# Performance work log

Measured on AMD Instinct MI355X. Metric: run time of the kernel, lower is better.

Reference implementation:

```python
import jax, jax.numpy as jnp
import numpy as np

D = 1024      # input_dim / hidden_size
H = 16        # n_heads
HD = D // H   # head_size = 64
F = 4096      # mlp_dim
EPS = 1e-6


def setup_inputs() -> dict:
    key = jax.random.key(0)
    ks = jax.random.split(key, 16)
    s = 0.02
    inp = {
        "x": jax.random.normal(ks[0], (4, 2048, D), dtype=jnp.float32),
        # attention params (torch Linear: y = x @ W.T + b; we store W as [out,in])
        "Wq": jax.random.normal(ks[1], (D, D), dtype=jnp.float32) * s,
        "bq": jax.random.normal(ks[2], (D,), dtype=jnp.float32) * s,
        "Wk": jax.random.normal(ks[3], (D, D), dtype=jnp.float32) * s,
        "bk": jax.random.normal(ks[4], (D,), dtype=jnp.float32) * s,
        "Wv": jax.random.normal(ks[5], (D, D), dtype=jnp.float32) * s,
        "bv": jax.random.normal(ks[6], (D,), dtype=jnp.float32) * s,
        "Wo": jax.random.normal(ks[7], (D, D), dtype=jnp.float32) * s,
        "bo": jax.random.normal(ks[8], (D,), dtype=jnp.float32) * s,
        # MLP params
        "W1": jax.random.normal(ks[9], (F, D), dtype=jnp.float32) * s,
        "b1": jax.random.normal(ks[10], (F,), dtype=jnp.float32) * s,
        "W2": jax.random.normal(ks[11], (D, F), dtype=jnp.float32) * s,
        "b2": jax.random.normal(ks[12], (D,), dtype=jnp.float32) * s,
        # LayerNorm params
        "ln1_g": jnp.ones((D,), dtype=jnp.float32),
        "ln1_b": jnp.zeros((D,), dtype=jnp.float32),
        "ln2_g": jnp.ones((D,), dtype=jnp.float32),
        "ln2_b": jnp.zeros((D,), dtype=jnp.float32),
    }
    return inp


def _layernorm(x, g, b):
    mu = jnp.mean(x, axis=-1, keepdims=True)
    var = jnp.mean(jnp.square(x - mu), axis=-1, keepdims=True)
    return (x - mu) * jax.lax.rsqrt(var + EPS) * g + b


def reference(x, Wq, bq, Wk, bk, Wv, bv, Wo, bo, W1, b1, W2, b2,
              ln1_g, ln1_b, ln2_g, ln2_b):
    B, S, _ = x.shape
    h = x
    xn = _layernorm(x, ln1_g, ln1_b)
    # Q/K/V projections -> [B, H, S, HD]
    def split_heads(t):
        return t.reshape(B, S, H, HD).transpose(0, 2, 1, 3)
    q = split_heads(xn @ Wq.T + bq)
    k = split_heads(xn @ Wk.T + bk)
    v = split_heads(xn @ Wv.T + bv)
    scores = jnp.einsum('bhqd,bhkd->bhqk', q, k) / np.sqrt(HD).astype(np.float32)
    probs = jax.nn.softmax(scores, axis=-1)
    ctx = jnp.einsum('bhqk,bhkd->bhqd', probs, v)      # [B,H,S,HD]
    ctx = ctx.transpose(0, 2, 1, 3).reshape(B, S, D)
    attn_out = ctx @ Wo.T + bo
    x = attn_out + h
    h = x
    xn = _layernorm(x, ln2_g, ln2_b)
    y = jax.nn.gelu(xn @ W1.T + b1, approximate=False)  # torch nn.GELU() = exact erf gelu
    y = y @ W2.T + b2
    return y + h
```

## Files before the change

### kernel.cpp

```cpp
#include <hip/hip_runtime.h>
#include <hip/hip_bf16.h>
#include <math.h>

typedef __attribute__((ext_vector_type(8))) short short8;
typedef __attribute__((ext_vector_type(4))) float f32x4;

#define MFMA_BF16 __builtin_amdgcn_mfma_f32_16x16x32_bf16

__device__ __forceinline__ ushort f2bf(float f) {
  union { __hip_bfloat16 h; ushort u; } c;
  c.h = __float2bfloat16(f);
  return c.u;
}
__device__ __forceinline__ void async_cp16(const ushort* g, ushort* l) {
  __builtin_amdgcn_global_load_lds(
      (const __attribute__((address_space(1))) void*)g,
      (__attribute__((address_space(3))) void*)l, 16, 0, 0);
}

__global__ __launch_bounds__(256) void conv_all(
    const float* __restrict__ Wq, const float* __restrict__ Wk,
    const float* __restrict__ Wv, const float* __restrict__ Wo,
    const float* __restrict__ W1, const float* __restrict__ W2,
    const float* __restrict__ bq, const float* __restrict__ bk,
    const float* __restrict__ bv,
    ushort* __restrict__ wqkv, ushort* __restrict__ wo,
    ushort* __restrict__ w1, ushort* __restrict__ w2,
    float* __restrict__ bqkv) {
  int i = blockIdx.x * 256 + threadIdx.x;
  if (i < 3145728) {
    const float* src; ushort* dst; int off;
    if (i < 786432)        {
      dst = wqkv; off = i;
      if (i < 262144)      src = Wq + (size_t)i * 4;
      else if (i < 524288) src = Wk + (size_t)(i - 262144) * 4;
      else                 src = Wv + (size_t)(i - 524288) * 4;
    } else if (i < 1048576) { dst = wo; off = i - 786432;  src = Wo + (size_t)off * 4; }
    else if (i < 2097152)   { dst = w1; off = i - 1048576; src = W1 + (size_t)off * 4; }
    else                    { dst = w2; off = i - 2097152; src = W2 + (size_t)off * 4; }
    float4 v = *(const float4*)src;
    ushort4 o;
    o.x = f2bf(v.x); o.y = f2bf(v.y); o.z = f2bf(v.z); o.w = f2bf(v.w);
    ((ushort4*)dst)[off] = o;
  } else if (i < 3146496) {
    int off = i - 3145728;
    const float* src;
    if (off < 256)      src = bq + (size_t)off * 4;
    else if (off < 512) src = bk + (size_t)(off - 256) * 4;
    else                src = bv + (size_t)(off - 512) * 4;
    ((float4*)bqkv)[off] = *(const float4*)src;
  }
}

__global__ __launch_bounds__(256) void ln_kernel(const float* __restrict__ x,
    const float* __restrict__ g, const float* __restrict__ b,
    ushort* __restrict__ out) {
  const int row = blockIdx.x, t = threadIdx.x;
  float4 v = ((const float4*)(x + (size_t)row * 1024))[t];
  float s  = v.x + v.y + v.z + v.w;
  float ss = v.x*v.x + v.y*v.y + v.z*v.z + v.w*v.w;
  #pragma unroll
  for (int off = 32; off >= 1; off >>= 1) {
    s  += __shfl_xor(s, off);
    ss += __shfl_xor(ss, off);
  }
  __shared__ float red[8];
  int wv = t >> 6, ln = t & 63;
  if (ln == 0) { red[wv] = s; red[4 + wv] = ss; }
  __syncthreads();
  float S  = red[0] + red[1] + red[2] + red[3];
  float SS = red[4] + red[5] + red[6] + red[7];
  float mu  = S * (1.0f/1024.0f);
  float var = SS * (1.0f/1024.0f) - mu*mu;
  float rs  = rsqrtf(var + 1e-6f);
  float4 gv = ((const float4*)g)[t];
  float4 bv = ((const float4*)b)[t];
  ushort4 o;
  o.x = f2bf((v.x-mu)*rs*gv.x + bv.x);
  o.y = f2bf((v.y-mu)*rs*gv.y + bv.y);
  o.z = f2bf((v.z-mu)*rs*gv.z + bv.z);
  o.w = f2bf((v.w-mu)*rs*gv.w + bv.w);
  ((ushort4*)(out + (size_t)row*1024))[t] = o;
}

enum { EPI_QK = 0, EPI_VT = 1, EPI_WO = 2, EPI_GELU = 3, EPI_OUT = 4 };

template <int EPI>
__global__ __launch_bounds__(256) void gemm_kernel(const ushort* __restrict__ A,
    const ushort* __restrict__ Bw, const float* __restrict__ bias,
    const float* __restrict__ res, void* __restrict__ outp,
    void* __restrict__ outp2, int K, int N, float scale) {
  __shared__ ushort As[2][128 * 32];
  __shared__ ushort Bs[2][128 * 32];
  const int t = threadIdx.x;
  const int m0 = blockIdx.x * 128, n0 = blockIdx.y * 128;
  const int lane = t & 63, wave = t >> 6;
  const int col = lane & 15, quad = lane >> 4;
  const int wrow = (wave >> 1) * 64, wcol = (wave & 1) * 64;

  f32x4 acc[4][4];
  #pragma unroll
  for (int i = 0; i < 4; i++)
    #pragma unroll
    for (int j = 0; j < 4; j++)
      acc[i][j] = (f32x4){0.f, 0.f, 0.f, 0.f};

  const int lrow = lane >> 2, lcol = (lane & 3) * 8;
  const ushort* Ag = A  + (size_t)(m0 + wave * 32 + lrow) * K + lcol;
  const ushort* Bg = Bw + (size_t)(n0 + wave * 32 + lrow) * K + lcol;
  const int ldso = (wave * 32) * 32;

  for (int k0 = 0; k0 < K; k0 += 64) {
    __syncthreads();
    #pragma unroll
    for (int c = 0; c < 2; c++) {
      async_cp16(Ag + k0 + c * 32,                  &As[c][ldso]);
      async_cp16(Ag + (size_t)16 * K + k0 + c * 32, &As[c][ldso + 16 * 32]);
      async_cp16(Bg + k0 + c * 32,                  &Bs[c][ldso]);
      async_cp16(Bg + (size_t)16 * K + k0 + c * 32, &Bs[c][ldso + 16 * 32]);
    }
    __syncthreads();
    #pragma unroll
    for (int c = 0; c < 2; c++) {
      short8 af[4], bf[4];
      #pragma unroll
      for (int tm = 0; tm < 4; tm++)
        af[tm] = *(const short8*)&As[c][(wrow + tm * 16 + col) * 32 + quad * 8];
      #pragma unroll
      for (int tn = 0; tn < 4; tn++)
        bf[tn] = *(const short8*)&Bs[c][(wcol + tn * 16 + col) * 32 + quad * 8];
      #pragma unroll
      for (int tm = 0; tm < 4; tm++)
        #pragma unroll
        for (int tn = 0; tn < 4; tn++)
          acc[tm][tn] = MFMA_BF16(af[tm], bf[tn], acc[tm][tn], 0, 0, 0);
    }
  }

  #pragma unroll
  for (int tm = 0; tm < 4; tm++) {
    #pragma unroll
    for (int tn = 0; tn < 4; tn++) {
      const int n = n0 + wcol + tn * 16 + col;
      const float bn = (EPI == EPI_VT) ? 0.f : bias[n];
      #pragma unroll
      for (int r = 0; r < 4; r++) {
        const int m = m0 + wrow + tm * 16 + quad * 4 + r;
        float v = acc[tm][tn][r] + bn;
        if (EPI == EPI_VT) {
          float vv = v + bias[m];
          int h = m >> 6, hd = m & 63, bb = n >> 11, s2 = n & 2047;
          ((ushort*)outp)[((size_t)((bb * 16 + h) * 64 + hd)) * 2048 + s2] = f2bf(vv);
        } else if (EPI == EPI_GELU) {
          float u = v * 0.7978845608028654f * (1.0f + 0.044715f * v * v);
          float e = __builtin_amdgcn_exp2f(u * 2.885390081777927f);
          float th = 1.0f - 2.0f * __builtin_amdgcn_rcpf(e + 1.0f);
          ((ushort*)outp)[(size_t)m * N + n] = f2bf(0.5f * v * (1.0f + th));
        } else {
          ((float*)outp)[(size_t)m * N + n] = v + res[(size_t)m * N + n];
        }
      }
    }
  }
}

template <int EPI>
__global__ __launch_bounds__(512, 2) void gemm256_kernel(const ushort* __restrict__ A,
    const ushort* __restrict__ Bw, const float* __restrict__ bias,
    void* __restrict__ outp, void* __restrict__ outp2, int K, int N, float scale) {
  __shared__ ushort As[2][256 * 64];
  __shared__ ushort Bs[2][256 * 64];
  const int t = threadIdx.x;
  const int lane = t & 63, wave = t >> 6;
  const int col = lane & 15, quad = lane >> 4;
  const int m0 = blockIdx.x * 256, n0 = blockIdx.y * 256;
  const int wm = wave >> 2, wn = wave & 3;

  f32x4 acc[8][4];
  #pragma unroll
  for (int i = 0; i < 8; i++)
    #pragma unroll
    for (int j = 0; j < 4; j++)
      acc[i][j] = (f32x4){0.f, 0.f, 0.f, 0.f};

  size_t aoff[4], boff[4];
  int sdst[4];
  #pragma unroll
  for (int i = 0; i < 4; i++) {
    int c = i * 512 + t;
    int row = c >> 3, p = c & 7;
    int gcol = (p ^ (row & 7)) * 8;
    aoff[i] = (size_t)(m0 + row) * K + gcol;
    boff[i] = (size_t)(n0 + row) * K + gcol;
    sdst[i] = c * 8;
  }

  const int NT = K >> 6;
  #pragma unroll
  for (int i = 0; i < 4; i++) {
    async_cp16(A  + aoff[i], &As[0][sdst[i]]);
    async_cp16(Bw + boff[i], &Bs[0][sdst[i]]);
  }

  int cur = 0;
  for (int kt = 0; kt < NT; kt++) {
    if (kt + 1 < NT) {
      const int nxt = cur ^ 1;
      const int ko = (kt + 1) << 6;
      #pragma unroll
      for (int i = 0; i < 4; i++) {
        async_cp16(A  + aoff[i] + ko, &As[nxt][sdst[i]]);
        async_cp16(Bw + boff[i] + ko, &Bs[nxt][sdst[i]]);
      }
      asm volatile("s_waitcnt vmcnt(8)" ::: "memory");
    } else {
      asm volatile("s_waitcnt vmcnt(0)" ::: "memory");
    }
    __builtin_amdgcn_sched_barrier(0);
    __builtin_amdgcn_s_barrier();
    __builtin_amdgcn_sched_barrier(0);

    #pragma unroll
    for (int c = 0; c < 2; c++) {
      short8 af[8], bf[4];
      #pragma unroll
      for (int tm = 0; tm < 8; tm++) {
        const int row = wm * 128 + tm * 16 + col;
        af[tm] = *(const short8*)&As[cur][row * 64 + ((c * 4 + quad) ^ (row & 7)) * 8];
      }
      #pragma unroll
      for (int tn = 0; tn < 4; tn++) {
        const int row = wn * 64 + tn * 16 + col;
        bf[tn] = *(const short8*)&Bs[cur][row * 64 + ((c * 4 + quad) ^ (row & 7)) * 8];
      }
      __builtin_amdgcn_s_setprio(1);
      #pragma unroll
      for (int tm = 0; tm < 8; tm++)
        #pragma unroll
        for (int tn = 0; tn < 4; tn++)
          acc[tm][tn] = MFMA_BF16(af[tm], bf[tn], acc[tm][tn], 0, 0, 0);
      __builtin_amdgcn_s_setprio(0);
    }

    asm volatile("s_waitcnt lgkmcnt(0)" ::: "memory");
    __builtin_amdgcn_sched_barrier(0);
    __builtin_amdgcn_s_barrier();
    cur ^= 1;
  }

  #pragma unroll
  for (int tm = 0; tm < 8; tm++) {
    #pragma unroll
    for (int tn = 0; tn < 4; tn++) {
      const int n = n0 + wn * 64 + tn * 16 + col;
      const float bn = bias[n];
      #pragma unroll
      for (int r = 0; r < 4; r++) {
        const int m = m0 + wm * 128 + tm * 16 + quad * 4 + r;
        float v = acc[tm][tn][r] + bn;
        if (EPI == EPI_QK) {
          int nl = n & 1023, h = nl >> 6, hd = nl & 63;
          int bb = m >> 11, s2 = m & 2047;
          if (n < 1024)
            ((ushort*)outp)[(((size_t)(bb * 16 + h) * 2048 + s2) * 64) + hd] = f2bf(v * scale);
          else
            ((ushort*)outp2)[(((size_t)(bb * 16 + h) * 2048 + s2) * 64) + hd] = f2bf(v);
        } else {
          float u = v * 0.7978845608028654f * (1.0f + 0.044715f * v * v);
          float e = __builtin_amdgcn_exp2f(u * 2.885390081777927f);
          float th = 1.0f - 2.0f * __builtin_amdgcn_rcpf(e + 1.0f);
          ((ushort*)outp)[(size_t)m * N + n] = f2bf(0.5f * v * (1.0f + th));
        }
      }
    }
  }
}

__global__ __launch_bounds__(256) void attn_kernel(const ushort* __restrict__ Qb,
    const ushort* __restrict__ Kb, const ushort* __restrict__ Vt,
    ushort* __restrict__ ctx) {
  const int lane = threadIdx.x & 63, wave = threadIdx.x >> 6;
  const int col = lane & 15, quad = lane >> 4;
  const int bx = blockIdx.x;
  const int bh = bx & 63;
  const int qt = bx >> 6;
  const int qbase = qt * 128 + wave * 32;
  const ushort* Qh = Qb + (size_t)bh * 2048 * 64;
  const ushort* Kh = Kb + (size_t)bh * 2048 * 64;
  const ushort* Vh = Vt + (size_t)bh * 64 * 2048;

  short8 qa[2][2];
  #pragma unroll
  for (int qg = 0; qg < 2; qg++) {
    const ushort* Qr = Qh + (size_t)(qbase + qg * 16 + col) * 64 + quad * 8;
    qa[qg][0] = *(const short8*)Qr;
    qa[qg][1] = *(const short8*)(Qr + 32);
  }

  f32x4 Ot[2][4];
  float l_part[2];
  #pragma unroll
  for (int qg = 0; qg < 2; qg++) {
    l_part[qg] = 0.f;
    #pragma unroll
    for (int dt = 0; dt < 4; dt++) Ot[qg][dt] = (f32x4){0.f, 0.f, 0.f, 0.f};
  }

  __shared__ ushort Ks[2][2][64 * 32];
  __shared__ ushort Vs[2][2][64 * 32];
  __shared__ ushort P_lds[4][2][16][64];

  const int lrow = lane >> 2;
  const int srow = wave * 16 + lrow;
  const int lcol = ((lane & 3) ^ ((srow >> 1) & 3)) * 8;
  const ushort* Kg = Kh + (size_t)srow * 64 + lcol;
  const ushort* Vg = Vh + (size_t)srow * 2048 + lcol;
  const int so = (wave * 16) * 32;

  const int kvswz = (col >> 1) & 3;
  const int pswz = col & 7;

  async_cp16(Kg,      &Ks[0][0][so]);
  async_cp16(Kg + 32, &Ks[0][1][so]);
  async_cp16(Vg,      &Vs[0][0][so]);
  async_cp16(Vg + 32, &Vs[0][1][so]);
  __syncthreads();

  int cur = 0;
  for (int kb = 0; kb < 2048; kb += 64) {
    if (kb + 64 < 2048) {
      const int nxt = cur ^ 1;
      async_cp16(Kg + (size_t)(kb + 64) * 64,      &Ks[nxt][0][so]);
      async_cp16(Kg + (size_t)(kb + 64) * 64 + 32, &Ks[nxt][1][so]);
      async_cp16(Vg + (kb + 64),                   &Vs[nxt][0][so]);
      async_cp16(Vg + (kb + 64) + 32,              &Vs[nxt][1][so]);
    }

    short8 kf[4][2], vf[4][2];
    #pragma unroll
    for (int kt = 0; kt < 4; kt++)
      #pragma unroll
      for (int c = 0; c < 2; c++)
        kf[kt][c] = *(const short8*)&Ks[cur][c][(kt * 16 + col) * 32 + (quad ^ kvswz) * 8];
    #pragma unroll
    for (int dt = 0; dt < 4; dt++)
      #pragma unroll
      for (int c = 0; c < 2; c++)
        vf[dt][c] = *(const short8*)&Vs[cur][c][(dt * 16 + col) * 32 + (quad ^ kvswz) * 8];

    #pragma unroll
    for (int qg = 0; qg < 2; qg++) {
      f32x4 s[4];
      __builtin_amdgcn_s_setprio(1);
      #pragma unroll
      for (int kt = 0; kt < 4; kt++) {
        s[kt] = (f32x4){0.f, 0.f, 0.f, 0.f};
        s[kt] = MFMA_BF16(kf[kt][0], qa[qg][0], s[kt], 0, 0, 0);
        s[kt] = MFMA_BF16(kf[kt][1], qa[qg][1], s[kt], 0, 0, 0);
      }
      __builtin_amdgcn_s_setprio(0);
      ushort(*P)[64] = P_lds[wave][qg];
      #pragma unroll
      for (int kt = 0; kt < 4; kt++) {
        float p0 = __builtin_amdgcn_exp2f(s[kt][0]);
        float p1 = __builtin_amdgcn_exp2f(s[kt][1]);
        float p2 = __builtin_amdgcn_exp2f(s[kt][2]);
        float p3 = __builtin_amdgcn_exp2f(s[kt][3]);
        l_part[qg] += (p0 + p1) + (p2 + p3);
        uint2 pk;
        asm("v_cvt_pk_bf16_f32 %0, %1, %2" : "=v"(pk.x) : "v"(p0), "v"(p1));
        asm("v_cvt_pk_bf16_f32 %0, %1, %2" : "=v"(pk.y) : "v"(p2), "v"(p3));
        *(uint2*)&P[col][(((2 * kt + (quad >> 1)) ^ pswz) * 8) + (quad & 1) * 4] = pk;
      }
    }
    #pragma unroll
    for (int qg = 0; qg < 2; qg++) {
      #pragma unroll
      for (int c = 0; c < 2; c++) {
        short8 pf = *(const short8*)&P_lds[wave][qg][col][((4 * c + quad) ^ pswz) * 8];
        __builtin_amdgcn_s_setprio(1);
        #pragma unroll
        for (int dt = 0; dt < 4; dt++)
          Ot[qg][dt] = MFMA_BF16(vf[dt][c], pf, Ot[qg][dt], 0, 0, 0);
        __builtin_amdgcn_s_setprio(0);
      }
    }
    __syncthreads();
    cur ^= 1;
  }

  const int bb = bh >> 4, h = bh & 15;
  #pragma unroll
  for (int qg = 0; qg < 2; qg++) {
    float l = l_part[qg];
    l += __shfl_xor(l, 16);
    l += __shfl_xor(l, 32);
    float inv = __builtin_amdgcn_rcpf(l);
    const int q = qbase + qg * 16 + col;
    size_t base = ((size_t)(bb * 2048 + q)) * 1024 + h * 64;
    #pragma unroll
    for (int dt = 0; dt < 4; dt++) {
      ushort4 o;
      o.x = f2bf(Ot[qg][dt][0] * inv);
      o.y = f2bf(Ot[qg][dt][1] * inv);
      o.z = f2bf(Ot[qg][dt][2] * inv);
      o.w = f2bf(Ot[qg][dt][3] * inv);
      *(ushort4*)&ctx[base + dt * 16 + quad * 4] = o;
    }
  }
}

extern "C" void kernel_launch(void* const* d_in, const int* in_sizes, int n_in,
                              void* d_out, int out_size, void* d_ws, size_t ws_size,
                              hipStream_t stream) {
  const float* x     = (const float*)d_in[0];
  const float* Wq    = (const float*)d_in[1];
  const float* bq    = (const float*)d_in[2];
  const float* Wk    = (const float*)d_in[3];
  const float* bk    = (const float*)d_in[4];
  const float* Wv    = (const float*)d_in[5];
  const float* bv    = (const float*)d_in[6];
  const float* Wo    = (const float*)d_in[7];
  const float* bo    = (const float*)d_in[8];
  const float* W1    = (const float*)d_in[9];
  const float* b1    = (const float*)d_in[10];
  const float* W2    = (const float*)d_in[11];
  const float* b2    = (const float*)d_in[12];
  const float* ln1_g = (const float*)d_in[13];
  const float* ln1_b = (const float*)d_in[14];
  const float* ln2_g = (const float*)d_in[15];
  const float* ln2_b = (const float*)d_in[16];

  const size_t MB = 1ull << 20;
  char* ws = (char*)d_ws;
  ushort* Wqkv_b = (ushort*)(ws + 0 * MB);
  ushort* Wo_b   = (ushort*)(ws + 6 * MB);
  ushort* W1_b   = (ushort*)(ws + 8 * MB);
  ushort* W2_b   = (ushort*)(ws + 16 * MB);
  ushort* xn1    = (ushort*)(ws + 24 * MB);
  ushort* Qb     = (ushort*)(ws + 40 * MB);
  ushort* Kb     = (ushort*)(ws + 56 * MB);
  ushort* Vt     = (ushort*)(ws + 72 * MB);
  ushort* ctxb   = (ushort*)(ws + 88 * MB);
  float*  x2     = (float*)(ws + 104 * MB);
  ushort* xn2    = (ushort*)(ws + 136 * MB);
  ushort* y1     = (ushort*)(ws + 152 * MB);
  float*  bqkv   = (float*)(ws + 152 * MB);

  conv_all<<<12291, 256, 0, stream>>>(Wq, Wk, Wv, Wo, W1, W2, bq, bk, bv,
                                      Wqkv_b, Wo_b, W1_b, W2_b, bqkv);

  ln_kernel<<<8192, 256, 0, stream>>>(x, ln1_g, ln1_b, xn1);

  const float cs = 0.125f * 1.4426950408889634f;
  gemm256_kernel<EPI_QK><<<dim3(32, 8), 512, 0, stream>>>(
      xn1, Wqkv_b, bqkv, Qb, Kb, 1024, 2048, cs);
  gemm_kernel<EPI_VT><<<dim3(8, 64), 256, 0, stream>>>(
      Wqkv_b + (size_t)2048 * 1024, xn1, bqkv + 2048, nullptr, Vt, nullptr,
      1024, 8192, 1.0f);

  attn_kernel<<<1024, 256, 0, stream>>>(Qb, Kb, Vt, ctxb);

  gemm_kernel<EPI_WO><<<dim3(64, 8), 256, 0, stream>>>(
      ctxb, Wo_b, bo, x, x2, nullptr, 1024, 1024, 1.0f);

  ln_kernel<<<8192, 256, 0, stream>>>(x2, ln2_g, ln2_b, xn2);

  gemm256_kernel<EPI_GELU><<<dim3(32, 16), 512, 0, stream>>>(
      xn2, W1_b, b1, y1, nullptr, 1024, 4096, 1.0f);
  gemm_kernel<EPI_OUT><<<dim3(64, 8), 256, 0, stream>>>(
      y1, W2_b, b2, x2, d_out, nullptr, 4096, 1024, 1.0f);
}
```

Baseline: 515.2 us.

## Replace 128x128 GEMMs with pipelined 256x128 tile kernel; load V directly from global

Adds a new 512-thread GEMM kernel with a 256x128 tile, XOR-swizzled LDS layout, double buffering that issues the next tile's async loads before computing the current one, and explicit waitcnt/barrier scheduling. It replaces the older 128x128 single-stage kernel for the V projection, the Wo projection and the W2 down-projection. The aim is more reuse per loaded byte and overlap of global loads with MFMA work. Separately, the attention kernel stops staging V through LDS and reads V fragments straight from global memory. That saves LDS traffic and barriers but risks global-load latency on the critical path.

```diff
diff --git a/kernel.cpp b/kernel.cpp
--- a/kernel.cpp
+++ b/kernel.cpp
@@ -86,85 +86,6 @@
 enum { EPI_QK = 0, EPI_VT = 1, EPI_WO = 2, EPI_GELU = 3, EPI_OUT = 4 };
 
 template <int EPI>
-__global__ __launch_bounds__(256) void gemm_kernel(const ushort* __restrict__ A,
-    const ushort* __restrict__ Bw, const float* __restrict__ bias,
-    const float* __restrict__ res, void* __restrict__ outp,
-    void* __restrict__ outp2, int K, int N, float scale) {
-  __shared__ ushort As[2][128 * 32];
-  __shared__ ushort Bs[2][128 * 32];
-  const int t = threadIdx.x;
-  const int m0 = blockIdx.x * 128, n0 = blockIdx.y * 128;
-  const int lane = t & 63, wave = t >> 6;
-  const int col = lane & 15, quad = lane >> 4;
-  const int wrow = (wave >> 1) * 64, wcol = (wave & 1) * 64;
-
-  f32x4 acc[4][4];
-  #pragma unroll
-  for (int i = 0; i < 4; i++)
-    #pragma unroll
-    for (int j = 0; j < 4; j++)
-      acc[i][j] = (f32x4){0.f, 0.f, 0.f, 0.f};
-
-  const int lrow = lane >> 2, lcol = (lane & 3) * 8;
-  const ushort* Ag = A  + (size_t)(m0 + wave * 32 + lrow) * K + lcol;
-  const ushort* Bg = Bw + (size_t)(n0 + wave * 32 + lrow) * K + lcol;
-  const int ldso = (wave * 32) * 32;
-
-  for (int k0 = 0; k0 < K; k0 += 64) {
-    __syncthreads();
-    #pragma unroll
-    for (int c = 0; c < 2; c++) {
-      async_cp16(Ag + k0 + c * 32,                  &As[c][ldso]);
-      async_cp16(Ag + (size_t)16 * K + k0 + c * 32, &As[c][ldso + 16 * 32]);
-      async_cp16(Bg + k0 + c * 32,                  &Bs[c][ldso]);
-      async_cp16(Bg + (size_t)16 * K + k0 + c * 32, &Bs[c][ldso + 16 * 32]);
-    }
-    __syncthreads();
-    #pragma unroll
-    for (int c = 0; c < 2; c++) {
-      short8 af[4], bf[4];
-      #pragma unroll
-      for (int tm = 0; tm < 4; tm++)
-        af[tm] = *(const short8*)&As[c][(wrow + tm * 16 + col) * 32 + quad * 8];
-      #pragma unroll
-      for (int tn = 0; tn < 4; tn++)
-        bf[tn] = *(const short8*)&Bs[c][(wcol + tn * 16 + col) * 32 + quad * 8];
-      #pragma unroll
-      for (int tm = 0; tm < 4; tm++)
-        #pragma unroll
-        for (int tn = 0; tn < 4; tn++)
-          acc[tm][tn] = MFMA_BF16(af[tm], bf[tn], acc[tm][tn], 0, 0, 0);
-    }
-  }
-
-  #pragma unroll
-  for (int tm = 0; tm < 4; tm++) {
-    #pragma unroll
-    for (int tn = 0; tn < 4; tn++) {
-      const int n = n0 + wcol + tn * 16 + col;
-      const float bn = (EPI == EPI_VT) ? 0.f : bias[n];
-      #pragma unroll
-      for (int r = 0; r < 4; r++) {
-        const int m = m0 + wrow + tm * 16 + quad * 4 + r;
-        float v = acc[tm][tn][r] + bn;
-        if (EPI == EPI_VT) {
-          float vv = v + bias[m];
-          int h = m >> 6, hd = m & 63, bb = n >> 11, s2 = n & 2047;
-          ((ushort*)outp)[((size_t)((bb * 16 + h) * 64 + hd)) * 2048 + s2] = f2bf(vv);
-        } else if (EPI == EPI_GELU) {
-          float u = v * 0.7978845608028654f * (1.0f + 0.044715f * v * v);
-          float e = __builtin_amdgcn_exp2f(u * 2.885390081777927f);
-          float th = 1.0f - 2.0f * __builtin_amdgcn_rcpf(e + 1.0f);
-          ((ushort*)outp)[(size_t)m * N + n] = f2bf(0.5f * v * (1.0f + th));
-        } else {
-          ((float*)outp)[(size_t)m * N + n] = v + res[(size_t)m * N + n];
-        }
-      }
-    }
-  }
-}
-
-template <int EPI>
 __global__ __launch_bounds__(512, 2) void gemm256_kernel(const ushort* __restrict__ A,
     const ushort* __restrict__ Bw, const float* __restrict__ bias,
     void* __restrict__ outp, void* __restrict__ outp2, int K, int N, float scale) {
@@ -276,6 +197,114 @@
   }
 }
 
+template <int EPI>
+__global__ __launch_bounds__(512, 2) void gemmBig_kernel(const ushort* __restrict__ A,
+    const ushort* __restrict__ Bw, const float* __restrict__ bias,
+    const float* __restrict__ res, void* __restrict__ outp, int K, int N) {
+  __shared__ ushort As[2][256 * 64];
+  __shared__ ushort Bs[2][128 * 64];
+  const int t = threadIdx.x;
+  const int lane = t & 63, wave = t >> 6;
+  const int col = lane & 15, quad = lane >> 4;
+  const int m0 = blockIdx.x * 256, n0 = blockIdx.y * 128;
+  const int wm = wave >> 1, wn = wave & 1;
+
+  f32x4 acc[4][4];
+  #pragma unroll
+  for (int i = 0; i < 4; i++)
+    #pragma unroll
+    for (int j = 0; j < 4; j++)
+      acc[i][j] = (f32x4){0.f, 0.f, 0.f, 0.f};
+
+  size_t aoff[4], boff[2];
+  int adst[4], bdst[2];
+  #pragma unroll
+  for (int i = 0; i < 4; i++) {
+    int c = i * 512 + t;
+    int row = c >> 3, p = c & 7;
+    aoff[i] = (size_t)(m0 + row) * K + (p ^ (row & 7)) * 8;
+    adst[i] = c * 8;
+  }
+  #pragma unroll
+  for (int i = 0; i < 2; i++) {
+    int c = i * 512 + t;
+    int row = c >> 3, p = c & 7;
+    boff[i] = (size_t)(n0 + row) * K + (p ^ (row & 7)) * 8;
+    bdst[i] = c * 8;
+  }
+
+  const int NT = K >> 6;
+  #pragma unroll
+  for (int i = 0; i < 4; i++) async_cp16(A + aoff[i], &As[0][adst[i]]);
+  #pragma unroll
+  for (int i = 0; i < 2; i++) async_cp16(Bw + boff[i], &Bs[0][bdst[i]]);
+
+  int cur = 0;
+  for (int kt = 0; kt < NT; kt++) {
+    if (kt + 1 < NT) {
+      const int nxt = cur ^ 1;
+      const int ko = (kt + 1) << 6;
+      #pragma unroll
+      for (int i = 0; i < 4; i++) async_cp16(A + aoff[i] + ko, &As[nxt][adst[i]]);
+      #pragma unroll
+      for (int i = 0; i < 2; i++) async_cp16(Bw + boff[i] + ko, &Bs[nxt][bdst[i]]);
+      asm volatile("s_waitcnt vmcnt(6)" ::: "memory");
+    } else {
+      asm volatile("s_waitcnt vmcnt(0)" ::: "memory");
+    }
+    __builtin_amdgcn_sched_barrier(0);
+    __builtin_amdgcn_s_barrier();
+    __builtin_amdgcn_sched_barrier(0);
+
+    #pragma unroll
+    for (int c = 0; c < 2; c++) {
+      short8 af[4], bf[4];
+      #pragma unroll
+      for (int tm = 0; tm < 4; tm++) {
+        const int row = wm * 64 + tm * 16 + col;
+        af[tm] = *(const short8*)&As[cur][row * 64 + ((c * 4 + quad) ^ (row & 7)) * 8];
+      }
+      #pragma unroll
+      for (int tn = 0; tn < 4; tn++) {
+        const int row = wn * 64 + tn * 16 + col;
+        bf[tn] = *(const short8*)&Bs[cur][row * 64 + ((c * 4 + quad) ^ (row & 7)) * 8];
+      }
+      __builtin_amdgcn_s_setprio(1);
+      #pragma unroll
+      for (int tm = 0; tm < 4; tm++)
+        #pragma unroll
+        for (int tn = 0; tn < 4; tn++)
+          acc[tm][tn] = MFMA_BF16(af[tm], bf[tn], acc[tm][tn], 0, 0, 0);
+      __builtin_amdgcn_s_setprio(0);
+    }
+
+    asm volatile("s_waitcnt lgkmcnt(0)" ::: "memory");
+    __builtin_amdgcn_sched_barrier(0);
+    __builtin_amdgcn_s_barrier();
+    cur ^= 1;
+  }
+
+  #pragma unroll
+  for (int tm = 0; tm < 4; tm++) {
+    #pragma unroll
+    for (int tn = 0; tn < 4; tn++) {
+      const int n = n0 + wn * 64 + tn * 16 + col;
+      #pragma unroll
+      for (int r = 0; r < 4; r++) {
+        const int m = m0 + wm * 64 + tm * 16 + quad * 4 + r;
+        float v = acc[tm][tn][r];
+        if (EPI == EPI_VT) {
+          float vv = v + bias[m];
+          int h = m >> 6, hd = m & 63, bb = n >> 11, s2 = n & 2047;
+          ((ushort*)outp)[((size_t)((bb * 16 + h) * 64 + hd)) * 2048 + s2] = f2bf(vv);
+        } else {
+          ((float*)outp)[(size_t)m * N + n] = v + bias[n] + res[(size_t)m * N + n];
+        }
+      }
+    }
+  }
+}
+
 __global__ __launch_bounds__(256) void attn_kernel(const ushort* __restrict__ Qb,
     const ushort* __restrict__ Kb, const ushort* __restrict__ Vt,
     ushort* __restrict__ ctx) {
@@ -307,23 +336,21 @@
   }
 
   __shared__ ushort Ks[2][2][64 * 32];
-  __shared__ ushort Vs[2][2][64 * 32];
   __shared__ ushort P_lds[4][2][16][64];
 
   const int lrow = lane >> 2;
   const int srow = wave * 16 + lrow;
   const int lcol = ((lane & 3) ^ ((srow >> 1) & 3)) * 8;
   const ushort* Kg = Kh + (size_t)srow * 64 + lcol;
-  const ushort* Vg = Vh + (size_t)srow * 2048 + lcol;
   const int so = (wave * 16) * 32;
 
   const int kvswz = (col >> 1) & 3;
   const int pswz = col & 7;
 
+  const ushort* Vl = Vh + (size_t)col * 2048 + quad * 8;
+
   async_cp16(Kg,      &Ks[0][0][so]);
   async_cp16(Kg + 32, &Ks[0][1][so]);
-  async_cp16(Vg,      &Vs[0][0][so]);
-  async_cp16(Vg + 32, &Vs[0][1][so]);
   __syncthreads();
 
   int cur = 0;
@@ -332,21 +359,21 @@
       const int nxt = cur ^ 1;
       async_cp16(Kg + (size_t)(kb + 64) * 64,      &Ks[nxt][0][so]);
       async_cp16(Kg + (size_t)(kb + 64) * 64 + 32, &Ks[nxt][1][so]);
-      async_cp16(Vg + (kb + 64),                   &Vs[nxt][0][so]);
-      async_cp16(Vg + (kb + 64) + 32,              &Vs[nxt][1][so]);
-    }
-
-    short8 kf[4][2], vf[4][2];
+    }
+
+    short8 vf[4][2];
+    #pragma unroll
+    for (int dt = 0; dt < 4; dt++)
+      #pragma unroll
+      for (int c = 0; c < 2; c++)
+        vf[dt][c] = *(const short8*)(Vl + (size_t)(dt * 16) * 2048 + kb + c * 32);
+
+    short8 kf[4][2];
     #pragma unroll
     for (int kt = 0; kt < 4; kt++)
       #pragma unroll
       for (int c = 0; c < 2; c++)
         kf[kt][c] = *(const short8*)&Ks[cur][c][(kt * 16 + col) * 32 + (quad ^ kvswz) * 8];
-    #pragma unroll
-    for (int dt = 0; dt < 4; dt++)
-      #pragma unroll
-      for (int c = 0; c < 2; c++)
-        vf[dt][c] = *(const short8*)&Vs[cur][c][(dt * 16 + col) * 32 + (quad ^ kvswz) * 8];
 
     #pragma unroll
     for (int qg = 0; qg < 2; qg++) {
@@ -455,19 +482,18 @@
   const float cs = 0.125f * 1.4426950408889634f;
   gemm256_kernel<EPI_QK><<<dim3(32, 8), 512, 0, stream>>>(
       xn1, Wqkv_b, bqkv, Qb, Kb, 1024, 2048, cs);
-  gemm_kernel<EPI_VT><<<dim3(8, 64), 256, 0, stream>>>(
-      Wqkv_b + (size_t)2048 * 1024, xn1, bqkv + 2048, nullptr, Vt, nullptr,
-      1024, 8192, 1.0f);
+  gemmBig_kernel<EPI_VT><<<dim3(4, 64), 512, 0, stream>>>(
+      Wqkv_b + (size_t)2048 * 1024, xn1, bqkv + 2048, nullptr, Vt, 1024, 8192);
 
   attn_kernel<<<1024, 256, 0, stream>>>(Qb, Kb, Vt, ctxb);
 
-  gemm_kernel<EPI_WO><<<dim3(64, 8), 256, 0, stream>>>(
-      ctxb, Wo_b, bo, x, x2, nullptr, 1024, 1024, 1.0f);
+  gemmBig_kernel<EPI_WO><<<dim3(32, 8), 512, 0, stream>>>(
+      ctxb, Wo_b, bo, x, x2, 1024, 1024);
 
   ln_kernel<<<8192, 256, 0, stream>>>(x2, ln2_g, ln2_b, xn2);
 
   gemm256_kernel<EPI_GELU><<<dim3(32, 16), 512, 0, stream>>>(
       xn2, W1_b, b1, y1, nullptr, 1024, 4096, 1.0f);
-  gemm_kernel<EPI_OUT><<<dim3(64, 8), 256, 0, stream>>>(
-      y1, W2_b, b2, x2, d_out, nullptr, 4096, 1024, 1.0f);
-}
+  gemmBig_kernel<EPI_OUT><<<dim3(32, 8), 512, 0, stream>>>(
+      y1, W2_b, b2, x2, d_out, 4096, 1024);
+}
```

Result: slower. 579.8 us (+12.5%).
